# Kernel optimization log

Hardware: AMD Instinct MI355X
Metric: run time of the kernel (lower is better)

Reference implementation:

```python
import jax, jax.numpy as jnp
import numpy as np

B, T, C, H = 2, 2048, 1024, 16


def setup_inputs() -> dict:
    key = jax.random.key(0)
    ks = jax.random.split(key, 9)
    s = 1.0 / np.sqrt(C)
    return {
        "query": jax.random.normal(ks[0], (B, T, C), dtype=jnp.float32),
        "Wq": jax.random.normal(ks[1], (C, C), dtype=jnp.float32) * s,
        "bq": jnp.zeros((C,), dtype=jnp.float32),
        "Wk": jax.random.normal(ks[2], (C, C), dtype=jnp.float32) * s,
        "bk": jnp.zeros((C,), dtype=jnp.float32),
        "Wv": jax.random.normal(ks[3], (C, C), dtype=jnp.float32) * s,
        "bv": jnp.zeros((C,), dtype=jnp.float32),
        "Wp": jax.random.normal(ks[4], (C, C), dtype=jnp.float32) * s,
        "bp": jnp.zeros((C,), dtype=jnp.float32),
        "n_head": H,
    }


def reference(query, Wq, bq, Wk, bk, Wv, bv, Wp, bp, n_head):
    b, t, c = query.shape
    d = c // n_head
    # QKV projections -> [b, h, t, d]
    q = (query @ Wq + bq).reshape(b, t, n_head, d).transpose(0, 2, 1, 3)
    k = (query @ Wk + bk).reshape(b, t, n_head, d).transpose(0, 2, 1, 3)
    v = (query @ Wv + bv).reshape(b, t, n_head, d).transpose(0, 2, 1, 3)
    scale = 1.0 / jnp.sqrt(jnp.asarray(d, dtype=query.dtype))
    att = jnp.einsum('bhtd,bhsd->bhts', q, k) * scale  # [b,h,t,t]
    causal = jnp.tril(jnp.ones((t, t), dtype=bool))
    att = jnp.where(causal[None, None, :, :], att, -jnp.inf)
    att = jax.nn.softmax(att, axis=-1)
    y = jnp.einsum('bhts,bhsd->bhtd', att, v)  # [b,h,t,d]
    y = y.transpose(0, 2, 1, 3).reshape(b, t, c)
    return y @ Wp + bp
```

## Files before the change

kernel.cpp:

```cpp
#include <hip/hip_runtime.h>
#include <math.h>

#define B_ 2
#define T_ 2048
#define C_ 1024
#define H_ 16
#define D_ 64
#define M_ (B_*T_)

typedef __bf16 bf16x8 __attribute__((ext_vector_type(8)));
typedef __bf16 bf16x4 __attribute__((ext_vector_type(4)));
typedef float  f32x4  __attribute__((ext_vector_type(4)));

__device__ __forceinline__ unsigned short f2bf(float f) {
    unsigned int u = __float_as_uint(f);
    u += 0x7FFFu + ((u >> 16) & 1u);
    return (unsigned short)(u >> 16);
}

__device__ __forceinline__ void gload16(const void* g, void* l) {
    __builtin_amdgcn_global_load_lds(
        (const __attribute__((address_space(1))) void*)g,
        (__attribute__((address_space(3))) void*)l, 16, 0, 0);
}

__global__ __launch_bounds__(256) void prep_kernel(
    const float* __restrict__ X, unsigned short* __restrict__ Xb,
    const float* __restrict__ W0, const float* __restrict__ W1,
    const float* __restrict__ W2, const float* __restrict__ W3,
    unsigned short* __restrict__ T0, unsigned short* __restrict__ T1,
    unsigned short* __restrict__ T2, unsigned short* __restrict__ T3)
{
    const int tid = threadIdx.x;
    if (blockIdx.x < 2048) {
        const size_t i = ((size_t)blockIdx.x * 256 + tid) * 8;
        const float4 a = *(const float4*)&X[i];
        const float4 b = *(const float4*)&X[i + 4];
        ushort4 s0, s1;
        s0.x = f2bf(a.x); s0.y = f2bf(a.y); s0.z = f2bf(a.z); s0.w = f2bf(a.w);
        s1.x = f2bf(b.x); s1.y = f2bf(b.y); s1.z = f2bf(b.z); s1.w = f2bf(b.w);
        *(ushort4*)&Xb[i]     = s0;
        *(ushort4*)&Xb[i + 4] = s1;
        return;
    }
    const int bz = blockIdx.x - 2048;
    const int z = bz >> 10, rem = bz & 1023;
    const float* W; unsigned short* Wt;
    switch (z) {
        case 0: W = W0; Wt = T0; break;
        case 1: W = W1; Wt = T1; break;
        case 2: W = W2; Wt = T2; break;
        default: W = W3; Wt = T3; break;
    }
    __shared__ unsigned short tile[32][33];
    const int k0 = (rem >> 5) * 32, n0 = (rem & 31) * 32;
    {
        const int r = tid >> 3, c = (tid & 7) * 4;
        const float4 v = *(const float4*)&W[(size_t)(k0 + r)*C_ + n0 + c];
        tile[c+0][r] = f2bf(v.x);
        tile[c+1][r] = f2bf(v.y);
        tile[c+2][r] = f2bf(v.z);
        tile[c+3][r] = f2bf(v.w);
    }
    __syncthreads();
    {
        const int r = tid >> 3, c = (tid & 7) * 4;
        ushort4 s;
        s.x = tile[r][c+0]; s.y = tile[r][c+1]; s.z = tile[r][c+2]; s.w = tile[r][c+3];
        *(ushort4*)&Wt[(size_t)(n0 + r)*C_ + k0 + c] = s;
    }
}

__global__ __launch_bounds__(256) void gemm_mfma_kernel(
    const unsigned short* __restrict__ A, const unsigned short* __restrict__ Bt,
    const float* __restrict__ b0, const float* __restrict__ b1,
    const float* __restrict__ b2,
    void* __restrict__ out0, void* __restrict__ out1, void* __restrict__ out2,
    int mode)
{
    __shared__ __align__(16) unsigned short Als[2][128 * 32];
    __shared__ __align__(16) unsigned short Bls[2][128 * 32];

    const int tid  = threadIdx.x;
    const int lane = tid & 63;
    const int wave = tid >> 6;
    const int wm = wave >> 1, wn = wave & 1;
    const int l15 = lane & 15, quad = lane >> 4;
    const int m0 = blockIdx.y * 128, n0 = blockIdx.x * 128;
    const int srow = lane >> 2;
    const int scol = (lane & 3) * 8;

    const f32x4 zero4 = {0.f, 0.f, 0.f, 0.f};
    f32x4 acc[4][4];
    #pragma unroll
    for (int i = 0; i < 4; ++i)
        #pragma unroll
        for (int j = 0; j < 4; ++j) acc[i][j] = zero4;

    for (int k0 = 0; k0 < C_; k0 += 64) {
        __syncthreads();
        #pragma unroll
        for (int h = 0; h < 2; ++h) {
            #pragma unroll
            for (int u = 0; u < 2; ++u) {
                const int r = wave*32 + u*16 + srow;
                gload16(&A [(size_t)(m0 + r)*C_ + k0 + h*32 + scol],
                        &Als[h][(wave*32 + u*16)*32]);
                gload16(&Bt[(size_t)(n0 + r)*C_ + k0 + h*32 + scol],
                        &Bls[h][(wave*32 + u*16)*32]);
            }
        }
        __syncthreads();

        #pragma unroll
        for (int h = 0; h < 2; ++h) {
            bf16x8 af[4], bfr[4];
            #pragma unroll
            for (int i = 0; i < 4; ++i)
                af[i] = *(const bf16x8*)&Als[h][(wm*64 + i*16 + l15)*32 + quad*8];
            #pragma unroll
            for (int j = 0; j < 4; ++j)
                bfr[j] = *(const bf16x8*)&Bls[h][(wn*64 + j*16 + l15)*32 + quad*8];

            #pragma unroll
            for (int i = 0; i < 4; ++i)
                #pragma unroll
                for (int j = 0; j < 4; ++j)
                    acc[i][j] = __builtin_amdgcn_mfma_f32_16x16x32_bf16(
                        af[i], bfr[j], acc[i][j], 0, 0, 0);
        }
    }

    if (mode == 0) {
        float* o0 = (float*)out0;
        #pragma unroll
        for (int j = 0; j < 4; ++j) {
            const int n = n0 + wn*64 + j*16 + l15;
            const float bias = b0[n];
            #pragma unroll
            for (int i = 0; i < 4; ++i)
                #pragma unroll
                for (int r = 0; r < 4; ++r) {
                    const int m = m0 + wm*64 + i*16 + quad*4 + r;
                    o0[(size_t)m*C_ + n] = acc[i][j][r] + bias;
                }
        }
        return;
    }

    __syncthreads();
    unsigned short* Ep = (wave < 2) ? &Als[wave][0] : &Bls[wave - 2][0];

    const int which = n0 >> 10;
    const int c0 = n0 & (C_ - 1);
    const int h  = (c0 >> 6) + wn;
    const int bb = m0 >> 11;
    const int t0 = (m0 & (T_ - 1)) + wm*64;
    const int bh = bb*H_ + h;
    const float* bp = (which == 0) ? b0 : (which == 1 ? b1 : b2);
    const float qscale = (which == 0) ? 0.125f : 1.0f;

    if (which < 2) {
        #pragma unroll
        for (int j = 0; j < 4; ++j) {
            const int cl = j*16 + l15;
            const float bias = bp[c0 + wn*64 + cl];
            #pragma unroll
            for (int i = 0; i < 4; ++i)
                #pragma unroll
                for (int r = 0; r < 4; ++r)
                    Ep[(i*16 + quad*4 + r)*64 + cl] =
                        f2bf((acc[i][j][r] + bias) * qscale);
        }
        unsigned short* op = (which == 0) ? (unsigned short*)out0
                                          : (unsigned short*)out1;
        const int chunk = lane & 7;
        #pragma unroll
        for (int u = 0; u < 8; ++u) {
            const int row = u*8 + (lane >> 3);
            const uint4 v = *(const uint4*)&Ep[row*64 + chunk*8];
            *(uint4*)&op[((size_t)bh*T_ + t0 + row)*D_ + chunk*8] = v;
        }
    } else {
        #pragma unroll
        for (int j = 0; j < 4; ++j) {
            const int cl = j*16 + l15;
            const float bias = bp[c0 + wn*64 + cl];
            const int xo = (l15 & 7) * 8;
            #pragma unroll
            for (int i = 0; i < 4; ++i) {
                ushort4 pk;
                pk.x = f2bf(acc[i][j][0] + bias);
                pk.y = f2bf(acc[i][j][1] + bias);
                pk.z = f2bf(acc[i][j][2] + bias);
                pk.w = f2bf(acc[i][j][3] + bias);
                *(ushort4*)&Ep[cl*64 + ((i*16 + quad*4) ^ xo)] = pk;
            }
        }
        unsigned short* op = (unsigned short*)out2;
        const int chunk = lane & 7;
        #pragma unroll
        for (int u = 0; u < 8; ++u) {
            const int d = u*8 + (lane >> 3);
            const uint4 v = *(const uint4*)&Ep[d*64 + ((chunk*8) ^ ((d & 7)*8))];
            *(uint4*)&op[((size_t)bh*D_ + d)*T_ + t0 + chunk*8] = v;
        }
    }
}

__global__ __launch_bounds__(256) void flash_mfma_kernel(
    const unsigned short* __restrict__ Qs, const unsigned short* __restrict__ Ks,
    const unsigned short* __restrict__ Vts, unsigned short* __restrict__ Y,
    float* __restrict__ parts, float* __restrict__ lbase)
{
    __shared__ __align__(16) unsigned short Kls[64 * 64];
    __shared__ __align__(16) unsigned short Vls[64 * 64];
    __shared__ __align__(16) unsigned short Pls[4 * 2048];

    const int tid  = threadIdx.x;
    const int lane = tid & 63, wave = tid >> 6;
    const int l15  = lane & 15, quad = lane >> 4;
    const int job  = blockIdx.x >> 5;
    const int bh   = blockIdx.x & 31;
    const bool isA = (job < 8);
    const int a    = isA ? job : job - 8;

    int qts[2], slos[2], shis[2], slots[2], nseg;
    if (isA) {
        qts[0] = a;      slos[0] = 0;        shis[0] = 2*a + 2;  slots[0] = -1;
        qts[1] = 15 - a; slos[1] = 0;        shis[1] = 15 - 2*a; slots[1] = 0;
        nseg = 2;
    } else {
        qts[0] = 15 - a; slos[0] = 15 - 2*a; shis[0] = 32 - 2*a; slots[0] = 1;
        nseg = 1;
    }

    unsigned short* Pw = &Pls[wave * 2048];
    const int kd_s = wave >> 1;
    const int c8_s = (kd_s * 4 + quad) * 8;
    const int b_ = bh >> 4, h_ = bh & (H_ - 1);
    const f32x4 zero4 = {0.f, 0.f, 0.f, 0.f};

    for (int sg = 0; sg < nseg; ++sg) {
        const int qt  = qts[sg];
        const int qw0 = qt * 128 + wave * 32;

        bf16x8 qf[2][2];
        #pragma unroll
        for (int i = 0; i < 2; ++i)
            #pragma unroll
            for (int kd = 0; kd < 2; ++kd)
                qf[i][kd] = *(const bf16x8*)&Qs[((size_t)bh*T_ + qw0 + i*16 + l15)*D_
                                                + kd*32 + quad*8];

        f32x4 o[2][4];
        #pragma unroll
        for (int i = 0; i < 2; ++i)
            #pragma unroll
            for (int jd = 0; jd < 4; ++jd) o[i][jd] = zero4;
        float lsum[2] = {0.f, 0.f};

        for (int it = slos[sg]; it < shis[sg]; ++it) {
            const int s0 = it * 64;
            __syncthreads();
            #pragma unroll
            for (int u = 0; u < 2; ++u) {
                const int cu  = 2*wave + u;
                const int row = ((cu & 3) << 4) + l15;
                gload16(&Ks [((size_t)bh*T_ + s0 + row)*D_ + c8_s],
                        (char*)Kls + cu*1024);
                gload16(&Vts[((size_t)bh*D_ + row)*T_ + s0 + c8_s],
                        (char*)Vls + cu*1024);
            }
            __syncthreads();

            if (s0 > qw0 + 31) continue;

            f32x4 st[2][4];
            #pragma unroll
            for (int i = 0; i < 2; ++i)
                #pragma unroll
                for (int j = 0; j < 4; ++j) st[i][j] = zero4;
            #pragma unroll
            for (int kd = 0; kd < 2; ++kd) {
                bf16x8 kf[4];
                #pragma unroll
                for (int j = 0; j < 4; ++j)
                    kf[j] = *(const bf16x8*)&Kls[lane*8 + j*512 + kd*2048];
                #pragma unroll
                for (int i = 0; i < 2; ++i)
                    #pragma unroll
                    for (int j = 0; j < 4; ++j)
                        st[i][j] = __builtin_amdgcn_mfma_f32_16x16x32_bf16(
                            kf[j], qf[i][kd], st[i][j], 0, 0, 0);
            }

            const bool diag = (s0 + 63 > qw0);
            #pragma unroll
            for (int i = 0; i < 2; ++i) {
                const int qrow = qw0 + i*16 + l15;
                #pragma unroll
                for (int j = 0; j < 4; ++j)
                    #pragma unroll
                    for (int r = 0; r < 4; ++r) {
                        float e = __expf(st[i][j][r]);
                        if (diag && (s0 + j*16 + quad*4 + r > qrow)) e = 0.f;
                        st[i][j][r] = e;
                        lsum[i] += e;
                    }
            }

            #pragma unroll
            for (int i = 0; i < 2; ++i)
                #pragma unroll
                for (int j = 0; j < 4; ++j) {
                    bf16x4 pk = {(__bf16)st[i][j][0], (__bf16)st[i][j][1],
                                 (__bf16)st[i][j][2], (__bf16)st[i][j][3]};
                    *(bf16x4*)&Pw[(((j>>1)*2 + i)*4 + (j&1)*2 + (quad>>1))*128
                                   + l15*8 + (quad&1)*4] = pk;
                }

            #pragma unroll
            for (int kk = 0; kk < 2; ++kk) {
                bf16x8 pf[2], vf[4];
                #pragma unroll
                for (int i = 0; i < 2; ++i)
                    pf[i] = *(const bf16x8*)&Pw[(kk*2 + i)*512 + lane*8];
                #pragma unroll
                for (int jd = 0; jd < 4; ++jd)
                    vf[jd] = *(const bf16x8*)&Vls[lane*8 + jd*512 + kk*2048];
                #pragma unroll
                for (int i = 0; i < 2; ++i)
                    #pragma unroll
                    for (int jd = 0; jd < 4; ++jd)
                        o[i][jd] = __builtin_amdgcn_mfma_f32_16x16x32_bf16(
                            vf[jd], pf[i], o[i][jd], 0, 0, 0);
            }
        }

        #pragma unroll
        for (int i = 0; i < 2; ++i) {
            float v = lsum[i];
            v += __shfl_xor(v, 16, 64);
            v += __shfl_xor(v, 32, 64);
            lsum[i] = v;
        }

        if (slots[sg] < 0) {
            #pragma unroll
            for (int i = 0; i < 2; ++i) {
                const float inv = 1.0f / lsum[i];
                const int t = qw0 + i*16 + l15;
                #pragma unroll
                for (int jd = 0; jd < 4; ++jd) {
                    bf16x4 pk = {(__bf16)(o[i][jd][0] * inv),
                                 (__bf16)(o[i][jd][1] * inv),
                                 (__bf16)(o[i][jd][2] * inv),
                                 (__bf16)(o[i][jd][3] * inv)};
                    *(bf16x4*)&Y[((size_t)(b_*T_ + t))*C_ + h_*D_ + jd*16 + quad*4]
                        = pk;
                }
            }
        } else {
            const int gpi = bh*16 + a*2 + slots[sg];
            float* Op = parts + (size_t)gpi*8192;
            float* Lp = lbase + gpi*128;
            #pragma unroll
            for (int i = 0; i < 2; ++i) {
                const int tl = wave*32 + i*16 + l15;
                if (quad == 0) Lp[tl] = lsum[i];
                #pragma unroll
                for (int jd = 0; jd < 4; ++jd)
                    *(f32x4*)&Op[(size_t)tl*64 + jd*16 + quad*4] = o[i][jd];
            }
        }
    }
}

__global__ __launch_bounds__(256) void merge_kernel(
    const float* __restrict__ parts, const float* __restrict__ lbase,
    unsigned short* __restrict__ Y)
{
    const int pair = blockIdx.x;
    const int bh = pair >> 3, p = pair & 7;
    const int qt = 15 - p;
    const int g0 = bh*16 + p*2;
    const float* O0 = parts + (size_t)g0*8192;
    const float* O1 = O0 + 8192;
    const float* L0 = lbase + g0*128;
    const float* L1 = L0 + 128;

    const int tid = threadIdx.x;
    const int r = tid >> 1, c0 = (tid & 1) * 32;
    const float inv = 1.0f / (L0[r] + L1[r]);
    const int b = bh >> 4, h = bh & (H_ - 1);
    const int t = qt*128 + r;
    #pragma unroll
    for (int k = 0; k < 8; ++k) {
        const f32x4 a  = *(const f32x4*)&O0[(size_t)r*64 + c0 + k*4];
        const f32x4 bb = *(const f32x4*)&O1[(size_t)r*64 + c0 + k*4];
        bf16x4 pk = {(__bf16)((a[0]+bb[0])*inv), (__bf16)((a[1]+bb[1])*inv),
                     (__bf16)((a[2]+bb[2])*inv), (__bf16)((a[3]+bb[3])*inv)};
        *(bf16x4*)&Y[((size_t)(b*T_ + t))*C_ + h*D_ + c0 + k*4] = pk;
    }
}

extern "C" void kernel_launch(void* const* d_in, const int* in_sizes, int n_in,
                              void* d_out, int out_size, void* d_ws, size_t ws_size,
                              hipStream_t stream) {
    const float* query = (const float*)d_in[0];
    const float* Wq = (const float*)d_in[1];
    const float* bq = (const float*)d_in[2];
    const float* Wk = (const float*)d_in[3];
    const float* bk = (const float*)d_in[4];
    const float* Wv = (const float*)d_in[5];
    const float* bv = (const float*)d_in[6];
    const float* Wp = (const float*)d_in[7];
    const float* bp = (const float*)d_in[8];
    float* out = (float*)d_out;

    char* ws = (char*)d_ws;
    unsigned short* qbf   = (unsigned short*)(ws);
    unsigned short* kbf   = (unsigned short*)(ws + 8388608);
    unsigned short* vtbf  = (unsigned short*)(ws + 16777216);
    unsigned short* WtP   = (unsigned short*)(ws + 25165824);
    unsigned short* WtQKV = (unsigned short*)(ws + 27262976);
    unsigned short* yb    = (unsigned short*)(ws + 33554432);
    unsigned short* qx    = (unsigned short*)(ws + 41943040);
    float* lbase = (float*)(ws + 27262976);
    float* parts = out;

    prep_kernel<<<6144, 256, 0, stream>>>(
        query, qx, Wq, Wk, Wv, Wp,
        WtQKV, WtQKV + (size_t)C_*C_, WtQKV + 2*(size_t)C_*C_, WtP);

    gemm_mfma_kernel<<<dim3(3*C_/128, M_/128), 256, 0, stream>>>(
        qx, WtQKV, bq, bk, bv, qbf, kbf, vtbf, 1);

    flash_mfma_kernel<<<512, 256, 0, stream>>>(qbf, kbf, vtbf, yb, parts, lbase);
    merge_kernel<<<256, 256, 0, stream>>>(parts, lbase, yb);

    gemm_mfma_kernel<<<dim3(C_/128, M_/128), 256, 0, stream>>>(
        yb, WtP, bp, bp, bp, out, nullptr, nullptr, 0);
}
```

Baseline: 207.5 us.

## Replace QKV projection GEMM with 256x256-tile, 512-thread multi-stage pipelined kernel

Adds a dedicated QKV GEMM kernel that uses 256x256 output tiles with 8 waves and a 4-buffer LDS ring. Tiles are filled via direct global-to-LDS loads, with explicit vmcnt waits and raised priority around the MFMA bursts. The epilogue writes Q (pre-scaled by 1/sqrt(d)) and K row-major per head, and V transposed, staged through LDS. The aim is more operand reuse per tile and better overlap of loads with MFMA work. In exchange the grid shrinks to 192 blocks, fewer than the CU count, and each block needs 128KB of LDS.

```diff
diff --git a/kernel.cpp b/kernel.cpp
--- a/kernel.cpp
+++ b/kernel.cpp
@@ -208,6 +208,156 @@
     }
 }
 
+__global__ __launch_bounds__(512, 2) void gemm256_qkv_kernel(
+    const unsigned short* __restrict__ A, const unsigned short* __restrict__ Bt,
+    const float* __restrict__ b0, const float* __restrict__ b1,
+    const float* __restrict__ b2,
+    unsigned short* __restrict__ outq, unsigned short* __restrict__ outk,
+    unsigned short* __restrict__ outv)
+{
+    __shared__ __align__(16) unsigned short lds[4 * 16384];
+
+    const int tid  = threadIdx.x;
+    const int lane = tid & 63;
+    const int wave = tid >> 6;
+    const int l15  = lane & 15, quad = lane >> 4;
+    const int wm   = wave >> 2, wn = wave & 3;
+    const int m0   = blockIdx.y * 256, n0 = blockIdx.x * 256;
+
+    const int lrow = lane >> 2;
+    const int csw  = ((lane & 3) ^ ((lane >> 3) & 3)) * 8;
+    const int sw8  = (quad ^ ((l15 >> 1) & 3)) * 8;
+
+#define STAGE(tt) do {                                                         \
+        const int bi_ = ((tt) & 3) << 14;                                      \
+        const int k0_ = (tt) << 5;                                             \
+        const int ra_ = m0 + wave*32 + lrow;                                   \
+        const int rb_ = n0 + wave*32 + lrow;                                   \
+        gload16(&A [(size_t)ra_*C_ + k0_ + csw],      &lds[bi_ + wave*1024]);  \
+        gload16(&Bt[(size_t)rb_*C_ + k0_ + csw],      &lds[bi_ + 8192 + wave*1024]); \
+        gload16(&A [(size_t)(ra_+16)*C_ + k0_ + csw], &lds[bi_ + wave*1024 + 512]);  \
+        gload16(&Bt[(size_t)(rb_+16)*C_ + k0_ + csw], &lds[bi_ + 8192 + wave*1024 + 512]); \
+    } while (0)
+
+    const f32x4 zero4 = {0.f, 0.f, 0.f, 0.f};
+    f32x4 acc[8][4];
+    #pragma unroll
+    for (int i = 0; i < 8; ++i)
+        #pragma unroll
+        for (int j = 0; j < 4; ++j) acc[i][j] = zero4;
+
+    STAGE(0); STAGE(1); STAGE(2);
+
+    for (int t = 0; t < 32; ++t) {
+        const int bi = (t & 3) << 14;
+        __builtin_amdgcn_s_barrier();
+        __builtin_amdgcn_sched_barrier(0);
+        if (t < 29) {
+            STAGE(t + 3);
+            asm volatile("s_waitcnt vmcnt(12)" ::: "memory");
+        } else if (t == 29) {
+            asm volatile("s_waitcnt vmcnt(8)" ::: "memory");
+        } else if (t == 30) {
+            asm volatile("s_waitcnt vmcnt(4)" ::: "memory");
+        } else {
+            asm volatile("s_waitcnt vmcnt(0)" ::: "memory");
+        }
+        __builtin_amdgcn_s_barrier();
+        __builtin_amdgcn_sched_barrier(0);
+
+        const unsigned short* Ab = &lds[bi];
+        const unsigned short* Bb = &lds[bi + 8192];
+
+        bf16x8 bfr[4], af[4];
+        #pragma unroll
+        for (int j = 0; j < 4; ++j)
+            bfr[j] = *(const bf16x8*)&Bb[(wn*64 + j*16 + l15)*32 + sw8];
+        #pragma unroll
+        for (int i = 0; i < 4; ++i)
+            af[i] = *(const bf16x8*)&Ab[(wm*128 + i*16 + l15)*32 + sw8];
+
+        __builtin_amdgcn_s_setprio(1);
+        #pragma unroll
+        for (int i = 0; i < 4; ++i)
+            #pragma unroll
+            for (int j = 0; j < 4; ++j)
+                acc[i][j] = __builtin_amdgcn_mfma_f32_16x16x32_bf16(
+                    af[i], bfr[j], acc[i][j], 0, 0, 0);
+        __builtin_amdgcn_s_setprio(0);
+
+        #pragma unroll
+        for (int i = 0; i < 4; ++i)
+            af[i] = *(const bf16x8*)&Ab[(wm*128 + 64 + i*16 + l15)*32 + sw8];
+
+        __builtin_amdgcn_s_setprio(1);
+        #pragma unroll
+        for (int i = 0; i < 4; ++i)
+            #pragma unroll
+            for (int j = 0; j < 4; ++j)
+                acc[4+i][j] = __builtin_amdgcn_mfma_f32_16x16x32_bf16(
+                    af[i], bfr[j], acc[4+i][j], 0, 0, 0);
+        __builtin_amdgcn_s_setprio(0);
+    }
+#undef STAGE
+
+    __syncthreads();
+
+    unsigned short* Ep = &lds[wave * 8192];
+    const int which = n0 >> 10;
+    const int c0 = (n0 & 1023) + wn * 64;
+    const int h  = c0 >> 6;
+    const int bb = m0 >> 11;
+    const int t0 = (m0 & (T_ - 1)) + wm * 128;
+    const int bh = bb * H_ + h;
+    const float* bp = (which == 0) ? b0 : (which == 1 ? b1 : b2);
+    const float qscale = (which == 0) ? 0.125f : 1.0f;
+
+    if (which < 2) {
+        __bf16* Eb = (__bf16*)Ep;
+        #pragma unroll
+        for (int j = 0; j < 4; ++j) {
+            const int cl = j*16 + l15;
+            const float bias = bp[c0 + cl];
+            #pragma unroll
+            for (int i = 0; i < 8; ++i)
+                #pragma unroll
+                for (int r = 0; r < 4; ++r)
+                    Eb[(i*16 + quad*4 + r)*64 + cl] =
+                        (__bf16)((acc[i][j][r] + bias) * qscale);
+        }
+        unsigned short* op = (which == 0) ? outq : outk;
+        const int row8 = lane >> 3, chunk = lane & 7;
+        #pragma unroll
+        for (int u = 0; u < 16; ++u) {
+            const int row = u*8 + row8;
+            const uint4 v = *(const uint4*)&Ep[row*64 + chunk*8];
+            *(uint4*)&op[((size_t)bh*T_ + t0 + row)*D_ + chunk*8] = v;
+        }
+    } else {
+        #pragma unroll
+        for (int j = 0; j < 4; ++j) {
+            const int cl = j*16 + l15;
+            const float bias = bp[c0 + cl];
+            const int xo = (cl & 7) * 8;
+            #pragma unroll
+            for (int i = 0; i < 8; ++i) {
+                bf16x4 pk = {(__bf16)(acc[i][j][0] + bias),
+                             (__bf16)(acc[i][j][1] + bias),
+                             (__bf16)(acc[i][j][2] + bias),
+                             (__bf16)(acc[i][j][3] + bias)};
+                *(bf16x4*)&Ep[cl*128 + ((i*16 + quad*4) ^ xo)] = pk;
+            }
+        }
+        const int d4 = lane >> 4, chunk = lane & 15;
+        #pragma unroll
+        for (int u = 0; u < 16; ++u) {
+            const int d = u*4 + d4;
+            const uint4 v = *(const uint4*)&Ep[d*128 + ((chunk*8) ^ ((d & 7)*8))];
+            *(uint4*)&outv[((size_t)bh*D_ + d)*T_ + t0 + chunk*8] = v;
+        }
+    }
+}
+
 __global__ __launch_bounds__(256) void flash_mfma_kernel(
     const unsigned short* __restrict__ Qs, const unsigned short* __restrict__ Ks,
     const unsigned short* __restrict__ Vts, unsigned short* __restrict__ Y,
@@ -434,8 +584,8 @@
         query, qx, Wq, Wk, Wv, Wp,
         WtQKV, WtQKV + (size_t)C_*C_, WtQKV + 2*(size_t)C_*C_, WtP);
 
-    gemm_mfma_kernel<<<dim3(3*C_/128, M_/128), 256, 0, stream>>>(
-        qx, WtQKV, bq, bk, bv, qbf, kbf, vtbf, 1);
+    gemm256_qkv_kernel<<<dim3(12, 16), 512, 0, stream>>>(
+        qx, WtQKV, bq, bk, bv, qbf, kbf, vtbf);
 
     flash_mfma_kernel<<<512, 256, 0, stream>>>(qbf, kbf, vtbf, yb, parts, lbase);
     merge_kernel<<<256, 256, 0, stream>>>(parts, lbase, yb);
```

Measured after the change: 201.8 us. -2.8%, faster.
